# Optimization experiments

Measured on AMD Instinct MI355X. Metric: run time of the kernel, lower is better.

The kernel has to match this reference:

```python
import jax, jax.numpy as jnp
import numpy as np

D_MODEL = 2048
N_HEADS = 16
HEAD_DIM = 128
WINDOW = 512
ROPE_BASE = 10000.0
B, N = 2, 2048
INNER = N_HEADS * HEAD_DIM


def setup_inputs() -> dict:
    key = jax.random.key(0)
    k1, k2, k3 = jax.random.split(key, 3)
    x = jax.random.normal(k1, (B, N, D_MODEL), dtype=jnp.float32)
    # torch nn.Linear stores weight as [out_features, in_features]
    w_qkv = jax.random.normal(k2, (3 * INNER, D_MODEL), dtype=jnp.float32) / np.sqrt(D_MODEL)
    w_o = jax.random.normal(k3, (D_MODEL, INNER), dtype=jnp.float32) / np.sqrt(INNER)
    return {"x": x, "w_qkv": w_qkv, "w_o": w_o}


def _rotate_half(t):
    t1, t2 = jnp.split(t, 2, axis=-1)
    return jnp.concatenate([-t2, t1], axis=-1)


def _rope(q, k, offset=0):
    # q, k: [B, H, N, D]; GPT-NeoX half-split rotary embedding
    D = q.shape[-1]
    inv_freq = 1.0 / (ROPE_BASE ** (jnp.arange(0, D, 2, dtype=jnp.float32) / D))
    pos = jnp.arange(q.shape[2], dtype=jnp.float32) + offset
    ang = pos[:, None] * inv_freq[None, :]                 # [N, D/2]
    cos = jnp.concatenate([jnp.cos(ang), jnp.cos(ang)], axis=-1)  # [N, D]
    sin = jnp.concatenate([jnp.sin(ang), jnp.sin(ang)], axis=-1)
    q_r = q * cos + _rotate_half(q) * sin
    k_r = k * cos + _rotate_half(k) * sin
    return q_r, k_r


def reference(x, w_qkv, w_o):
    Bq, Nq, _ = x.shape
    # QKV projection (no bias)
    qkv = jnp.einsum('bnd,ed->bne', x, w_qkv)              # [B, N, 3*INNER]
    q, k, v = jnp.split(qkv, 3, axis=-1)
    def to_heads(t):
        return t.reshape(Bq, Nq, N_HEADS, HEAD_DIM).transpose(0, 2, 1, 3)  # [B,H,N,D]
    q, k, v = to_heads(q), to_heads(k), to_heads(v)
    q, k = _rope(q, k, offset=0)
    # sliding-window causal mask: valid key j for query i iff (i - WINDOW) < j <= i
    i = jnp.arange(Nq)[:, None]
    j = jnp.arange(Nq)[None, :]
    valid = (j > i - WINDOW) & (j <= i)                    # [N, N]
    scale = 1.0 / np.sqrt(HEAD_DIM)
    scores = jnp.einsum('bhnd,bhkd->bhnk', q, k) * scale   # [B,H,N,N]
    scores = jnp.where(valid[None, None], scores, -jnp.inf)
    att = jax.nn.softmax(scores, axis=-1)
    out = jnp.einsum('bhnk,bhkd->bhnd', att, v)
    out = out.transpose(0, 2, 1, 3).reshape(Bq, Nq, INNER)
    y = jnp.einsum('bni,di->bnd', out, w_o)
    return y
```

## Files before the change

### kernel.cpp

```cpp
#include <hip/hip_runtime.h>
#include <hip/hip_bf16.h>
#include <cstdint>

typedef __bf16 bf16x8 __attribute__((ext_vector_type(8)));
typedef float floatx4 __attribute__((ext_vector_type(4)));

__device__ __forceinline__ void gl2lds16(const void* g, void* l) {
  __builtin_amdgcn_global_load_lds(
      (const __attribute__((address_space(1))) unsigned int*)g,
      (__attribute__((address_space(3))) unsigned int*)(uintptr_t)l,
      16, 0, 0);
}

__global__ __launch_bounds__(256)
void cvt_kernel(const float* __restrict__ in, __hip_bfloat16* __restrict__ out, int n) {
  int i = (blockIdx.x * 256 + threadIdx.x) * 4;
  if (i >= n) return;
  const float4 v = *(const float4*)(in + i);
  out[i + 0] = __float2bfloat16(v.x);
  out[i + 1] = __float2bfloat16(v.y);
  out[i + 2] = __float2bfloat16(v.z);
  out[i + 3] = __float2bfloat16(v.w);
}


#define GEMM_PREAMBLE(APTR, BPTR)                                              \
  const int tid = threadIdx.x, lane = tid & 63, wave = tid >> 6;               \
  const int wr = wave >> 2, wc = wave & 3;                                     \
  const int m0 = blockIdx.x << 8, n0 = blockIdx.y << 8;                        \
  const int lrow = lane & 15, dg = lane >> 4, lq4 = dg * 4;                    \
  const int rslot = (dg ^ ((lrow >> 1) & 3)) * 8;                              \
  const int arow = tid >> 2;                                                   \
  const int ascol = ((tid & 3) ^ ((tid >> 3) & 3)) * 8;                        \
  const __hip_bfloat16* aS0 = (APTR) + (size_t)(m0 + arow) * 2048 + ascol;     \
  const __hip_bfloat16* aS1 = (APTR) + (size_t)(m0 + 128 + arow) * 2048 + ascol; \
  const __hip_bfloat16* bS0 = (BPTR) + (size_t)(n0 + arow) * 2048 + ascol;     \
  const __hip_bfloat16* bS1 = (BPTR) + (size_t)(n0 + 128 + arow) * 2048 + ascol; \
  floatx4 acc[8][4] = {};

#define STAGE_A(TT) do { const int bb_ = (TT) & 3; const int kk_ = (TT) * 32;  \
    gl2lds16(aS0 + kk_, &sm[bb_ * 16384 + tid * 8]);                           \
    gl2lds16(aS1 + kk_, &sm[bb_ * 16384 + 4096 + tid * 8]); } while (0)
#define STAGE_B(TT) do { const int bb_ = (TT) & 3; const int kk_ = (TT) * 32;  \
    gl2lds16(bS0 + kk_, &sm[bb_ * 16384 + 8192 + tid * 8]);                    \
    gl2lds16(bS1 + kk_, &sm[bb_ * 16384 + 12288 + tid * 8]); } while (0)

#define STAGE_AB(TT) do { STAGE_A(TT); STAGE_B(TT); } while (0)

#define MEMFENCE asm volatile("" ::: "memory")

#define KSTEP(TT, WIMM, DOSTAGE) do {                                          \
    const int bb = (TT) & 3;                                                   \
    MEMFENCE; __builtin_amdgcn_s_waitcnt(WIMM); MEMFENCE;                      \
    __builtin_amdgcn_s_barrier();            \
    MEMFENCE;                                                                  \
    bf16x8 af0[4], af1[4], bfr[4];                                             \
    _Pragma("unroll")                                                          \
    for (int mt = 0; mt < 4; mt++)                                             \
      af0[mt] = *(const bf16x8*)&sm[bb * 16384 + (wr * 128 + mt * 16 + lrow) * 32 + rslot]; \
    _Pragma("unroll")                                                          \
    for (int nt = 0; nt < 4; nt++)                                             \
      bfr[nt] = *(const bf16x8*)&sm[bb * 16384 + 8192 + (wc * 64 + nt * 16 + lrow) * 32 + rslot]; \
    if (DOSTAGE) STAGE_A((TT) + 3);                                            \
    MEMFENCE; __builtin_amdgcn_s_barrier(); MEMFENCE;                          \
    __builtin_amdgcn_s_waitcnt(0xC07F); MEMFENCE;                              \
    __builtin_amdgcn_s_setprio(1);                                             \
    _Pragma("unroll")                                                          \
    for (int mt = 0; mt < 4; mt++)                                             \
      _Pragma("unroll")                                                        \
      for (int nt = 0; nt < 4; nt++)                                           \
        acc[mt][nt] = __builtin_amdgcn_mfma_f32_16x16x32_bf16(af0[mt], bfr[nt], acc[mt][nt], 0, 0, 0); \
    __builtin_amdgcn_s_setprio(0);                                             \
    MEMFENCE; __builtin_amdgcn_s_barrier(); MEMFENCE;                          \
    _Pragma("unroll")                                                          \
    for (int mt = 0; mt < 4; mt++)                                             \
      af1[mt] = *(const bf16x8*)&sm[bb * 16384 + (wr * 128 + 64 + mt * 16 + lrow) * 32 + rslot]; \
    if (DOSTAGE) STAGE_B((TT) + 3);                                            \
    MEMFENCE; __builtin_amdgcn_s_barrier(); MEMFENCE;                          \
    __builtin_amdgcn_s_waitcnt(0xC07F); MEMFENCE;                              \
    __builtin_amdgcn_s_setprio(1);                                             \
    _Pragma("unroll")                                                          \
    for (int mt = 0; mt < 4; mt++)                                             \
      _Pragma("unroll")                                                        \
      for (int nt = 0; nt < 4; nt++)                                           \
        acc[4 + mt][nt] = __builtin_amdgcn_mfma_f32_16x16x32_bf16(af1[mt], bfr[nt], acc[4 + mt][nt], 0, 0, 0); \
    __builtin_amdgcn_s_setprio(0);                                             \
  } while (0)

#define GEMM_KLOOP()                                                           \
  STAGE_AB(0); STAGE_AB(1); STAGE_AB(2);                                       \
  for (int t = 0; t < 61; ++t) KSTEP(t, 0x0078, true);                         \
  KSTEP(61, 0x0078, false);                                                    \
  KSTEP(62, 0x0074, false);                                                    \
  KSTEP(63, 0x0070, false);

__global__ __launch_bounds__(512, 2)
void gemm_qkv256(const __hip_bfloat16* __restrict__ A,
                 const __hip_bfloat16* __restrict__ W,
                 __hip_bfloat16* __restrict__ Qr,
                 __hip_bfloat16* __restrict__ Kr,
                 __hip_bfloat16* __restrict__ Vt)
{
  extern __shared__ __hip_bfloat16 sm[];
  GEMM_PREAMBLE(A, W)
  GEMM_KLOOP()

  const int seg = n0 >> 11;
  const int h0 = (n0 & 2047) >> 7;
  const int b = m0 >> 11;
  const int seq0 = m0 & 2047;
  float* invfp = (float*)((char*)sm + 122880);

  __syncthreads();
  if (seg < 2 && tid < 64) invfp[tid] = __expf(-(float)tid * 0.14391156831212787f);

  const float qs = (seg == 0) ? 0.08838834764831845f : 1.0f;
  for (int p = 0; p < 2; ++p) {
    if (p) __syncthreads();
    if (wr == p) {
      if (seg < 2) {
#pragma unroll
        for (int mt = 0; mt < 8; mt++)
#pragma unroll
          for (int nt = 0; nt < 4; nt++)
#pragma unroll
            for (int r = 0; r < 4; r++)
              sm[(mt * 16 + lq4 + r) * 264 + wc * 64 + nt * 16 + lrow] =
                  __float2bfloat16(acc[mt][nt][r]);
      } else {
#pragma unroll
        for (int mt = 0; mt < 8; mt++)
#pragma unroll
          for (int nt = 0; nt < 4; nt++)
#pragma unroll
            for (int r = 0; r < 4; r++)
              sm[(wc * 64 + nt * 16 + lrow) * 136 + mt * 16 + lq4 + r] =
                  __float2bfloat16(acc[mt][nt][r]);
      }
    }
    __syncthreads();
    if (seg < 2) {
      __hip_bfloat16* Out = seg ? Kr : Qr;
#pragma unroll
      for (int it = 0; it < 4; ++it) {
        const int task = tid + it * 512;
        const int row = task >> 4;
        const int hh = (task >> 3) & 1;
        const int g8 = (task & 7) * 8;
        const int seq = seq0 + p * 128 + row;
        const float pos = (float)seq;
        const bf16x8 lo8 = *(const bf16x8*)&sm[row * 264 + hh * 128 + g8];
        const bf16x8 hi8 = *(const bf16x8*)&sm[row * 264 + hh * 128 + g8 + 64];
        alignas(16) __hip_bfloat16 lo[8], hi[8];
#pragma unroll
        for (int k = 0; k < 8; k++) {
          float sn, cs;
          __sincosf(pos * invfp[g8 + k], &sn, &cs);
          const float a = (float)lo8[k];
          const float bb2 = (float)hi8[k];
          lo[k] = __float2bfloat16((a * cs - bb2 * sn) * qs);
          hi[k] = __float2bfloat16((bb2 * cs + a * sn) * qs);
        }
        const size_t ob = ((size_t)((b * 16 + h0 + hh) * 2048 + seq)) * 128;
        *(bf16x8*)&Out[ob + g8] = *(const bf16x8*)lo;
        *(bf16x8*)&Out[ob + g8 + 64] = *(const bf16x8*)hi;
      }
    } else {
#pragma unroll
      for (int it = 0; it < 8; ++it) {
        const int task = tid + it * 512;
        const int col = task >> 4;
        const int sg = (task & 15) * 8;
        const bf16x8 v8 = *(const bf16x8*)&sm[col * 136 + sg];
        const int hh = col >> 7, d = col & 127;
        *(bf16x8*)&Vt[((size_t)((b * 16 + h0 + hh) * 128 + d)) * 2048 + seq0 + p * 128 + sg] = v8;
      }
    }
  }
}

__global__ __launch_bounds__(512, 2)
void gemm_o256(const __hip_bfloat16* __restrict__ A,
               const __hip_bfloat16* __restrict__ Wo,
               float* __restrict__ C)
{
  extern __shared__ __hip_bfloat16 sm[];
  GEMM_PREAMBLE(A, Wo)
  GEMM_KLOOP()
#pragma unroll
  for (int mt = 0; mt < 8; mt++)
#pragma unroll
    for (int nt = 0; nt < 4; nt++)
#pragma unroll
      for (int r = 0; r < 4; r++)
        C[(size_t)(m0 + wr * 128 + mt * 16 + lq4 + r) * 2048 +
          (n0 + wc * 64 + nt * 16 + lrow)] = acc[mt][nt][r];
}

#undef KSTEP
#undef GEMM_KLOOP
#undef STAGE_A
#undef STAGE_B
#undef STAGE_AB
#undef GEMM_PREAMBLE

#define KSTR 136
#define VSTR 72
__global__ __launch_bounds__(512, 4)
void attn_swa(const __hip_bfloat16* __restrict__ Qr, const __hip_bfloat16* __restrict__ Kr,
              const __hip_bfloat16* __restrict__ Vt, __hip_bfloat16* __restrict__ Out)
{
  __shared__ __hip_bfloat16 Ks[64 * KSTR];
  __shared__ __hip_bfloat16 Vs[128 * VSTR];
  __shared__ __hip_bfloat16 Pb[8][16 * VSTR];
  const int qt = blockIdx.x, bh = blockIdx.y;
  const int tid = threadIdx.x, lane = tid & 63, wave = tid >> 6;
  const int lrow = lane & 15, lk = (lane >> 4) * 8, lq4 = (lane >> 4) * 4;
  const int i0 = qt * 128;
  const float NEG_INF = -__builtin_inff();
  const __hip_bfloat16* Qh = Qr + (size_t)bh * 2048 * 128;
  const __hip_bfloat16* Kh = Kr + (size_t)bh * 2048 * 128;
  const __hip_bfloat16* Vh = Vt + (size_t)bh * 128 * 2048;

  const int ck0 = tid, ck1 = tid + 512;
  const int kr0 = ck0 >> 4, kg0 = (ck0 & 15) * 8;
  const int kr1 = ck1 >> 4, kg1 = (ck1 & 15) * 8;
  const int cv0 = tid, cv1 = tid + 512;
  const int vd0 = cv0 >> 3, vc0 = (cv0 & 7) * 8;
  const int vd1 = cv1 >> 3, vc1 = (cv1 & 7) * 8;

  const int iw = i0 + wave * 16 + lrow;
  bf16x8 qf[4];
#pragma unroll
  for (int ks = 0; ks < 4; ks++)
    qf[ks] = *(const bf16x8*)&Qh[(size_t)iw * 128 + ks * 32 + lk];

  floatx4 accO[8] = {};
  float m_i = NEG_INF, l_i = 0.f;
  const int imin = i0 + wave * 16;
  const int lo = i0 - 511;
  const int jt_lo = (lo > 0 ? lo : 0) >> 6;
  const int jt_hi = (i0 + 127) >> 6;

  int j0n = jt_lo * 64;
  int4 rk0 = *(const int4*)&Kh[(size_t)(j0n + kr0) * 128 + kg0];
  int4 rk1 = *(const int4*)&Kh[(size_t)(j0n + kr1) * 128 + kg1];
  int4 rv0 = *(const int4*)&Vh[(size_t)vd0 * 2048 + j0n + vc0];
  int4 rv1 = *(const int4*)&Vh[(size_t)vd1 * 2048 + j0n + vc1];

  for (int jt = jt_lo; jt <= jt_hi; jt++) {
    const int j0 = jt * 64;
    __syncthreads();
    *(int4*)&Ks[kr0 * KSTR + kg0] = rk0;
    *(int4*)&Ks[kr1 * KSTR + kg1] = rk1;
    *(int4*)&Vs[vd0 * VSTR + vc0] = rv0;
    *(int4*)&Vs[vd1 * VSTR + vc1] = rv1;
    if (jt < jt_hi) {
      const int jn = j0 + 64;
      rk0 = *(const int4*)&Kh[(size_t)(jn + kr0) * 128 + kg0];
      rk1 = *(const int4*)&Kh[(size_t)(jn + kr1) * 128 + kg1];
      rv0 = *(const int4*)&Vh[(size_t)vd0 * 2048 + jn + vc0];
      rv1 = *(const int4*)&Vh[(size_t)vd1 * 2048 + jn + vc1];
    }
    asm volatile("" ::: "memory");
    __builtin_amdgcn_s_waitcnt(0xC07F);
    __builtin_amdgcn_s_barrier();
    asm volatile("" ::: "memory");

    floatx4 s[4] = {};
#pragma unroll
    for (int nt = 0; nt < 4; nt++) {
      const int krow = (nt * 16 + lrow) * KSTR;
#pragma unroll
      for (int ks = 0; ks < 4; ks++) {
        const bf16x8 kf = *(const bf16x8*)&Ks[krow + ks * 32 + lk];
        s[nt] = __builtin_amdgcn_mfma_f32_16x16x32_bf16(kf, qf[ks], s[nt], 0, 0, 0);
      }
    }
    const bool full = (j0 + 63 <= imin) && (j0 >= imin + 15 - 511);
    float rmax = NEG_INF;
    if (full) {
#pragma unroll
      for (int nt = 0; nt < 4; nt++)
#pragma unroll
        for (int r = 0; r < 4; r++) rmax = fmaxf(rmax, s[nt][r]);
    } else {
#pragma unroll
      for (int nt = 0; nt < 4; nt++) {
#pragma unroll
        for (int r = 0; r < 4; r++) {
          const int j = j0 + nt * 16 + lq4 + r;
          const float sv = ((j <= iw) && (j > iw - 512)) ? s[nt][r] : NEG_INF;
          s[nt][r] = sv;
          rmax = fmaxf(rmax, sv);
        }
      }
    }
    rmax = fmaxf(rmax, __shfl_xor(rmax, 16));
    rmax = fmaxf(rmax, __shfl_xor(rmax, 32));
    const float mnew = fmaxf(m_i, rmax);
    const float alpha = __expf(fminf(m_i - mnew, 0.f));
    m_i = mnew;
    float rs = 0.f;
    if (full) {
#pragma unroll
      for (int nt = 0; nt < 4; nt++)
#pragma unroll
        for (int r = 0; r < 4; r++) {
          const float p = __expf(s[nt][r] - mnew);
          s[nt][r] = p;
          rs += p;
        }
    } else {
#pragma unroll
      for (int nt = 0; nt < 4; nt++)
#pragma unroll
        for (int r = 0; r < 4; r++) {
          const float sv = s[nt][r];
          const float p = (sv == NEG_INF) ? 0.f : __expf(sv - mnew);
          s[nt][r] = p;
          rs += p;
        }
    }
    rs += __shfl_xor(rs, 16);
    rs += __shfl_xor(rs, 32);
    l_i = l_i * alpha + rs;
#pragma unroll
    for (int dt = 0; dt < 8; dt++) accO[dt] *= alpha;
#pragma unroll
    for (int nt = 0; nt < 4; nt++) {
      alignas(8) __hip_bfloat16 p4[4];
#pragma unroll
      for (int r = 0; r < 4; r++) p4[r] = __float2bfloat16(s[nt][r]);
      *(uint64_t*)&Pb[wave][lrow * VSTR + nt * 16 + lq4] = *(const uint64_t*)p4;
    }
    bf16x8 pf[2];
#pragma unroll
    for (int jf = 0; jf < 2; jf++)
      pf[jf] = *(const bf16x8*)&Pb[wave][lrow * VSTR + jf * 32 + lk];
#pragma unroll
    for (int dt = 0; dt < 8; dt++) {
      const int vrow = (dt * 16 + lrow) * VSTR;
#pragma unroll
      for (int jf = 0; jf < 2; jf++) {
        const bf16x8 vf = *(const bf16x8*)&Vs[vrow + jf * 32 + lk];
        accO[dt] = __builtin_amdgcn_mfma_f32_16x16x32_bf16(vf, pf[jf], accO[dt], 0, 0, 0);
      }
    }
  }
  const int b = bh >> 4, h = bh & 15;
  const float inv_l = 1.0f / l_i;
  const size_t rowb = ((size_t)(b * 2048 + iw)) * 2048 + h * 128;
#pragma unroll
  for (int dt = 0; dt < 8; dt++) {
    alignas(8) __hip_bfloat16 o4[4];
#pragma unroll
    for (int r = 0; r < 4; r++) o4[r] = __float2bfloat16(accO[dt][r] * inv_l);
    *(uint64_t*)&Out[rowb + dt * 16 + lq4] = *(const uint64_t*)o4;
  }
}

extern "C" void kernel_launch(void* const* d_in, const int* in_sizes, int n_in,
                              void* d_out, int out_size, void* d_ws, size_t ws_size,
                              hipStream_t stream)
{
  const float* x = (const float*)d_in[0];
  const float* w_qkv = (const float*)d_in[1];
  const float* w_o = (const float*)d_in[2];
  float* y = (float*)d_out;
  char* ws = (char*)d_ws;

  const size_t SZ_X = 16777216;
  const size_t SZ_WQKV = 25165824;
  const size_t SZ_Q = 16777216;

  __hip_bfloat16* xb = (__hip_bfloat16*)(ws);
  __hip_bfloat16* wqkvb = (__hip_bfloat16*)(ws + SZ_X);
  __hip_bfloat16* Qr = (__hip_bfloat16*)(ws + SZ_X + SZ_WQKV);
  __hip_bfloat16* Kr = (__hip_bfloat16*)(ws + SZ_X + SZ_WQKV + SZ_Q);
  __hip_bfloat16* Vt = (__hip_bfloat16*)(ws + SZ_X + SZ_WQKV + 2 * SZ_Q);

  static bool s_attr_done = false;
  if (!s_attr_done) {
    hipFuncSetAttribute((const void*)gemm_qkv256,
                        hipFuncAttributeMaxDynamicSharedMemorySize, 131072);
    hipFuncSetAttribute((const void*)gemm_o256,
                        hipFuncAttributeMaxDynamicSharedMemorySize, 131072);
    s_attr_done = true;
  }

  cvt_kernel<<<dim3(8192), dim3(256), 0, stream>>>(x, xb, 8388608);
  cvt_kernel<<<dim3(12288), dim3(256), 0, stream>>>(w_qkv, wqkvb, 12582912);
  gemm_qkv256<<<dim3(16, 24), dim3(512), 131072, stream>>>(xb, wqkvb, Qr, Kr, Vt);
  attn_swa<<<dim3(16, 32), dim3(512), 0, stream>>>(Qr, Kr, Vt, xb );
  cvt_kernel<<<dim3(4096), dim3(256), 0, stream>>>(w_o, wqkvb, 4194304);
  gemm_o256<<<dim3(16, 8), dim3(512), 131072, stream>>>(xb, wqkvb, y);
}
```

Baseline: 361.2 us.

## Restructure GEMM k-steps, shrink output-GEMM tile, fuse input conversions

The QKV GEMM k-step now uses a single barrier per step: it issues the next stage's loads right after the barrier, then loads all eight A fragments and runs 32 MFMAs, instead of splitting the work into two halves with four barriers. The output GEMM uses 256x128 tiles with 3-load staging and 96KB LDS, which doubles the grid from 128 to 256 blocks so more CUs are busy. The two fp32-to-bf16 conversions of x and w_qkv are merged into one launch, relying on the two outputs being contiguous in the workspace. In exchange, holding more fragments raises register pressure, and dropping barriers may reduce overlap or risk an LDS race on the 4-deep buffer.

After: 338.9 us. -6.2%, faster.

```diff
diff --git a/kernel.cpp b/kernel.cpp
--- a/kernel.cpp
+++ b/kernel.cpp
@@ -23,76 +23,20 @@
   out[i + 3] = __float2bfloat16(v.w);
 }
 
-
-#define GEMM_PREAMBLE(APTR, BPTR)                                              \
-  const int tid = threadIdx.x, lane = tid & 63, wave = tid >> 6;               \
-  const int wr = wave >> 2, wc = wave & 3;                                     \
-  const int m0 = blockIdx.x << 8, n0 = blockIdx.y << 8;                        \
-  const int lrow = lane & 15, dg = lane >> 4, lq4 = dg * 4;                    \
-  const int rslot = (dg ^ ((lrow >> 1) & 3)) * 8;                              \
-  const int arow = tid >> 2;                                                   \
-  const int ascol = ((tid & 3) ^ ((tid >> 3) & 3)) * 8;                        \
-  const __hip_bfloat16* aS0 = (APTR) + (size_t)(m0 + arow) * 2048 + ascol;     \
-  const __hip_bfloat16* aS1 = (APTR) + (size_t)(m0 + 128 + arow) * 2048 + ascol; \
-  const __hip_bfloat16* bS0 = (BPTR) + (size_t)(n0 + arow) * 2048 + ascol;     \
-  const __hip_bfloat16* bS1 = (BPTR) + (size_t)(n0 + 128 + arow) * 2048 + ascol; \
-  floatx4 acc[8][4] = {};
-
-#define STAGE_A(TT) do { const int bb_ = (TT) & 3; const int kk_ = (TT) * 32;  \
-    gl2lds16(aS0 + kk_, &sm[bb_ * 16384 + tid * 8]);                           \
-    gl2lds16(aS1 + kk_, &sm[bb_ * 16384 + 4096 + tid * 8]); } while (0)
-#define STAGE_B(TT) do { const int bb_ = (TT) & 3; const int kk_ = (TT) * 32;  \
-    gl2lds16(bS0 + kk_, &sm[bb_ * 16384 + 8192 + tid * 8]);                    \
-    gl2lds16(bS1 + kk_, &sm[bb_ * 16384 + 12288 + tid * 8]); } while (0)
-
-#define STAGE_AB(TT) do { STAGE_A(TT); STAGE_B(TT); } while (0)
+__global__ __launch_bounds__(256)
+void cvt2_kernel(const float* __restrict__ in0, const float* __restrict__ in1,
+                 __hip_bfloat16* __restrict__ out, int n0, int ntot) {
+  int i = (blockIdx.x * 256 + threadIdx.x) * 4;
+  if (i >= ntot) return;
+  const float4 v = (i < n0) ? *(const float4*)(in0 + i)
+                            : *(const float4*)(in1 + (i - n0));
+  out[i + 0] = __float2bfloat16(v.x);
+  out[i + 1] = __float2bfloat16(v.y);
+  out[i + 2] = __float2bfloat16(v.z);
+  out[i + 3] = __float2bfloat16(v.w);
+}
 
 #define MEMFENCE asm volatile("" ::: "memory")
-
-#define KSTEP(TT, WIMM, DOSTAGE) do {                                          \
-    const int bb = (TT) & 3;                                                   \
-    MEMFENCE; __builtin_amdgcn_s_waitcnt(WIMM); MEMFENCE;                      \
-    __builtin_amdgcn_s_barrier();            \
-    MEMFENCE;                                                                  \
-    bf16x8 af0[4], af1[4], bfr[4];                                             \
-    _Pragma("unroll")                                                          \
-    for (int mt = 0; mt < 4; mt++)                                             \
-      af0[mt] = *(const bf16x8*)&sm[bb * 16384 + (wr * 128 + mt * 16 + lrow) * 32 + rslot]; \
-    _Pragma("unroll")                                                          \
-    for (int nt = 0; nt < 4; nt++)                                             \
-      bfr[nt] = *(const bf16x8*)&sm[bb * 16384 + 8192 + (wc * 64 + nt * 16 + lrow) * 32 + rslot]; \
-    if (DOSTAGE) STAGE_A((TT) + 3);                                            \
-    MEMFENCE; __builtin_amdgcn_s_barrier(); MEMFENCE;                          \
-    __builtin_amdgcn_s_waitcnt(0xC07F); MEMFENCE;                              \
-    __builtin_amdgcn_s_setprio(1);                                             \
-    _Pragma("unroll")                                                          \
-    for (int mt = 0; mt < 4; mt++)                                             \
-      _Pragma("unroll")                                                        \
-      for (int nt = 0; nt < 4; nt++)                                           \
-        acc[mt][nt] = __builtin_amdgcn_mfma_f32_16x16x32_bf16(af0[mt], bfr[nt], acc[mt][nt], 0, 0, 0); \
-    __builtin_amdgcn_s_setprio(0);                                             \
-    MEMFENCE; __builtin_amdgcn_s_barrier(); MEMFENCE;                          \
-    _Pragma("unroll")                                                          \
-    for (int mt = 0; mt < 4; mt++)                                             \
-      af1[mt] = *(const bf16x8*)&sm[bb * 16384 + (wr * 128 + 64 + mt * 16 + lrow) * 32 + rslot]; \
-    if (DOSTAGE) STAGE_B((TT) + 3);                                            \
-    MEMFENCE; __builtin_amdgcn_s_barrier(); MEMFENCE;                          \
-    __builtin_amdgcn_s_waitcnt(0xC07F); MEMFENCE;                              \
-    __builtin_amdgcn_s_setprio(1);                                             \
-    _Pragma("unroll")                                                          \
-    for (int mt = 0; mt < 4; mt++)                                             \
-      _Pragma("unroll")                                                        \
-      for (int nt = 0; nt < 4; nt++)                                           \
-        acc[4 + mt][nt] = __builtin_amdgcn_mfma_f32_16x16x32_bf16(af1[mt], bfr[nt], acc[4 + mt][nt], 0, 0, 0); \
-    __builtin_amdgcn_s_setprio(0);                                             \
-  } while (0)
-
-#define GEMM_KLOOP()                                                           \
-  STAGE_AB(0); STAGE_AB(1); STAGE_AB(2);                                       \
-  for (int t = 0; t < 61; ++t) KSTEP(t, 0x0078, true);                         \
-  KSTEP(61, 0x0078, false);                                                    \
-  KSTEP(62, 0x0074, false);                                                    \
-  KSTEP(63, 0x0070, false);
 
 __global__ __launch_bounds__(512, 2)
 void gemm_qkv256(const __hip_bfloat16* __restrict__ A,
@@ -102,8 +46,53 @@
                  __hip_bfloat16* __restrict__ Vt)
 {
   extern __shared__ __hip_bfloat16 sm[];
-  GEMM_PREAMBLE(A, W)
-  GEMM_KLOOP()
+  const int tid = threadIdx.x, lane = tid & 63, wave = tid >> 6;
+  const int wr = wave >> 2, wc = wave & 3;
+  const int m0 = blockIdx.x << 8, n0 = blockIdx.y << 8;
+  const int lrow = lane & 15, dg = lane >> 4, lq4 = dg * 4;
+  const int rslot = (dg ^ ((lrow >> 1) & 3)) * 8;
+  const int arow = tid >> 2;
+  const int ascol = ((tid & 3) ^ ((tid >> 3) & 3)) * 8;
+  const __hip_bfloat16* aS0 = A + (size_t)(m0 + arow) * 2048 + ascol;
+  const __hip_bfloat16* aS1 = A + (size_t)(m0 + 128 + arow) * 2048 + ascol;
+  const __hip_bfloat16* bS0 = W + (size_t)(n0 + arow) * 2048 + ascol;
+  const __hip_bfloat16* bS1 = W + (size_t)(n0 + 128 + arow) * 2048 + ascol;
+  floatx4 acc[8][4] = {};
+
+#define QSTAGE(TT) do { const int bb_ = (TT) & 3; const int kk_ = (TT) * 32;   \
+    gl2lds16(aS0 + kk_, &sm[bb_ * 16384 + tid * 8]);                           \
+    gl2lds16(aS1 + kk_, &sm[bb_ * 16384 + 4096 + tid * 8]);                    \
+    gl2lds16(bS0 + kk_, &sm[bb_ * 16384 + 8192 + tid * 8]);                    \
+    gl2lds16(bS1 + kk_, &sm[bb_ * 16384 + 12288 + tid * 8]); } while (0)
+
+#define QKSTEP(TT, WIMM, DOSTAGE) do {                                         \
+    MEMFENCE; __builtin_amdgcn_s_waitcnt(WIMM); MEMFENCE;                      \
+    __builtin_amdgcn_s_barrier(); MEMFENCE;                                    \
+    const int bb = (TT) & 3;                                                   \
+    if (DOSTAGE) QSTAGE((TT) + 3);                                             \
+    bf16x8 af[8], bfr[4];                                                      \
+    _Pragma("unroll")                                                          \
+    for (int mt = 0; mt < 8; mt++)                                             \
+      af[mt] = *(const bf16x8*)&sm[bb * 16384 + (wr * 128 + mt * 16 + lrow) * 32 + rslot]; \
+    _Pragma("unroll")                                                          \
+    for (int nt = 0; nt < 4; nt++)                                             \
+      bfr[nt] = *(const bf16x8*)&sm[bb * 16384 + 8192 + (wc * 64 + nt * 16 + lrow) * 32 + rslot]; \
+    __builtin_amdgcn_s_setprio(1);                                             \
+    _Pragma("unroll")                                                          \
+    for (int mt = 0; mt < 8; mt++)                                             \
+      _Pragma("unroll")                                                        \
+      for (int nt = 0; nt < 4; nt++)                                           \
+        acc[mt][nt] = __builtin_amdgcn_mfma_f32_16x16x32_bf16(af[mt], bfr[nt], acc[mt][nt], 0, 0, 0); \
+    __builtin_amdgcn_s_setprio(0);                                             \
+  } while (0)
+
+  QSTAGE(0); QSTAGE(1); QSTAGE(2);
+  for (int t = 0; t < 61; ++t) QKSTEP(t, 0x0078, true);
+  QKSTEP(61, 0x0078, false);
+  QKSTEP(62, 0x0074, false);
+  QKSTEP(63, 0x0070, false);
+#undef QKSTEP
+#undef QSTAGE
 
   const int seg = n0 >> 11;
   const int h0 = (n0 & 2047) >> 7;
@@ -185,24 +174,61 @@
                float* __restrict__ C)
 {
   extern __shared__ __hip_bfloat16 sm[];
-  GEMM_PREAMBLE(A, Wo)
-  GEMM_KLOOP()
+  const int tid = threadIdx.x, lane = tid & 63, wave = tid >> 6;
+  const int wr = wave >> 2, wc = wave & 3;
+  const int m0 = blockIdx.x << 8, n0 = blockIdx.y << 7;
+  const int lrow = lane & 15, dg = lane >> 4, lq4 = dg * 4;
+  const int rslot = (dg ^ ((lrow >> 1) & 3)) * 8;
+  const int arow = tid >> 2;
+  const int ascol = ((tid & 3) ^ ((tid >> 3) & 3)) * 8;
+  const __hip_bfloat16* aS0 = A + (size_t)(m0 + arow) * 2048 + ascol;
+  const __hip_bfloat16* aS1 = A + (size_t)(m0 + 128 + arow) * 2048 + ascol;
+  const __hip_bfloat16* bS0 = Wo + (size_t)(n0 + arow) * 2048 + ascol;
+  floatx4 acc[8][2] = {};
+
+#define OSTAGE(TT) do { const int bb_ = (TT) & 3; const int kk_ = (TT) * 32;   \
+    gl2lds16(aS0 + kk_, &sm[bb_ * 12288 + tid * 8]);                           \
+    gl2lds16(aS1 + kk_, &sm[bb_ * 12288 + 4096 + tid * 8]);                    \
+    gl2lds16(bS0 + kk_, &sm[bb_ * 12288 + 8192 + tid * 8]); } while (0)
+
+#define OKSTEP(TT, WIMM, DOSTAGE) do {                                         \
+    MEMFENCE; __builtin_amdgcn_s_waitcnt(WIMM); MEMFENCE;                      \
+    __builtin_amdgcn_s_barrier(); MEMFENCE;                                    \
+    const int bb = (TT) & 3;                                                   \
+    if (DOSTAGE) OSTAGE((TT) + 3);                                             \
+    bf16x8 af[8], bfr[2];                                                      \
+    _Pragma("unroll")                                                          \
+    for (int mt = 0; mt < 8; mt++)                                             \
+      af[mt] = *(const bf16x8*)&sm[bb * 12288 + (wr * 128 + mt * 16 + lrow) * 32 + rslot]; \
+    _Pragma("unroll")                                                          \
+    for (int nt = 0; nt < 2; nt++)                                             \
+      bfr[nt] = *(const bf16x8*)&sm[bb * 12288 + 8192 + (wc * 32 + nt * 16 + lrow) * 32 + rslot]; \
+    __builtin_amdgcn_s_setprio(1);                                             \
+    _Pragma("unroll")                                                          \
+    for (int mt = 0; mt < 8; mt++)                                             \
+      _Pragma("unroll")                                                        \
+      for (int nt = 0; nt < 2; nt++)                                           \
+        acc[mt][nt] = __builtin_amdgcn_mfma_f32_16x16x32_bf16(af[mt], bfr[nt], acc[mt][nt], 0, 0, 0); \
+    __builtin_amdgcn_s_setprio(0);                                             \
+  } while (0)
+
+  OSTAGE(0); OSTAGE(1); OSTAGE(2);
+  for (int t = 0; t < 61; ++t) OKSTEP(t, 0x0076, true);
+  OKSTEP(61, 0x0076, false);
+  OKSTEP(62, 0x0073, false);
+  OKSTEP(63, 0x0070, false);
+#undef OKSTEP
+#undef OSTAGE
+
 #pragma unroll
   for (int mt = 0; mt < 8; mt++)
 #pragma unroll
-    for (int nt = 0; nt < 4; nt++)
+    for (int nt = 0; nt < 2; nt++)
 #pragma unroll
       for (int r = 0; r < 4; r++)
         C[(size_t)(m0 + wr * 128 + mt * 16 + lq4 + r) * 2048 +
-          (n0 + wc * 64 + nt * 16 + lrow)] = acc[mt][nt][r];
-}
-
-#undef KSTEP
-#undef GEMM_KLOOP
-#undef STAGE_A
-#undef STAGE_B
-#undef STAGE_AB
-#undef GEMM_PREAMBLE
+          (n0 + wc * 32 + nt * 16 + lrow)] = acc[mt][nt][r];
+}
 
 #define KSTR 136
 #define VSTR 72
@@ -385,14 +411,13 @@
     hipFuncSetAttribute((const void*)gemm_qkv256,
                         hipFuncAttributeMaxDynamicSharedMemorySize, 131072);
     hipFuncSetAttribute((const void*)gemm_o256,
-                        hipFuncAttributeMaxDynamicSharedMemorySize, 131072);
+                        hipFuncAttributeMaxDynamicSharedMemorySize, 98304);
     s_attr_done = true;
   }
 
-  cvt_kernel<<<dim3(8192), dim3(256), 0, stream>>>(x, xb, 8388608);
-  cvt_kernel<<<dim3(12288), dim3(256), 0, stream>>>(w_qkv, wqkvb, 12582912);
+  cvt2_kernel<<<dim3(20480), dim3(256), 0, stream>>>(x, w_qkv, xb, 8388608, 20971520);
   gemm_qkv256<<<dim3(16, 24), dim3(512), 131072, stream>>>(xb, wqkvb, Qr, Kr, Vt);
   attn_swa<<<dim3(16, 32), dim3(512), 0, stream>>>(Qr, Kr, Vt, xb );
   cvt_kernel<<<dim3(4096), dim3(256), 0, stream>>>(w_o, wqkvb, 4194304);
-  gemm_o256<<<dim3(16, 8), dim3(512), 131072, stream>>>(xb, wqkvb, y);
-}
+  gemm_o256<<<dim3(16, 16), dim3(512), 98304, stream>>>(xb, wqkvb, y);
+}
```
